# Kernel optimization log

Hardware: AMD Instinct MI355X
Metric: run time of the kernel (lower is better)

## Reference

```python
import jax, jax.numpy as jnp
import numpy as np

# CIN config: input_dim (num_fields) = 32, cross_layer_sizes = [128, 128, 128], split_half = True
NUM_FIELDS = 32
EMBED_DIM = 16
BATCH = 4096
CROSS_SIZES = [128, 128, 128]


def setup_inputs() -> dict:
    key = jax.random.key(0)
    ks = jax.random.split(key, 8)
    x = jax.random.normal(ks[0], (BATCH, NUM_FIELDS, EMBED_DIM), dtype=jnp.float32)
    # Conv1d(kernel_size=1) weights: (out_ch, in_ch) + bias (out_ch,)
    prev = NUM_FIELDS
    inp = {"x": x}
    for i, cs in enumerate(CROSS_SIZES):
        in_ch = NUM_FIELDS * prev
        scale = 1.0 / np.sqrt(in_ch)
        inp[f"W{i}"] = jax.random.uniform(ks[1 + 2 * i], (cs, in_ch), dtype=jnp.float32, minval=-scale, maxval=scale)
        inp[f"b{i}"] = jax.random.uniform(ks[2 + 2 * i], (cs,), dtype=jnp.float32, minval=-scale, maxval=scale)
        prev = cs // 2  # split_half (applied after all but last, but prev for next conv uses halved size)
    return inp


def _cin_forward(x, Ws, bs):
    # x: (B, F, E)
    x0 = x
    h = x
    xs = []
    n_layers = len(Ws)
    for i in range(n_layers):
        B, F, E = x0.shape
        G = h.shape[1]
        # outer product over field dims -> (B, F*G, E)
        z = (x0[:, :, None, :] * h[:, None, :, :]).reshape(B, F * G, E)
        # 1x1 conv == channel matmul; bias broadcast over embed dim; relu
        y = jax.nn.relu(jnp.einsum('oc,bce->boe', Ws[i], z) + bs[i][None, :, None])
        if i != n_layers - 1:
            half = y.shape[1] // 2
            x_keep, h = y[:, :half, :], y[:, half:, :]
        else:
            x_keep, h = y, y
        xs.append(x_keep)
    return jnp.sum(jnp.concatenate(xs, axis=1), axis=2)  # (B, fc_input_dim)


def reference(x, W0, b0, W1, b1, W2, b2):
    return _cin_forward(x, [W0, W1, W2], [b0, b1, b2])
```

## Files before the change

kernel.cpp:

```cpp
#include <hip/hip_runtime.h>

typedef _Float16 half_t;
typedef _Float16 v8h __attribute__((ext_vector_type(8)));
typedef _Float16 v4h __attribute__((ext_vector_type(4)));
typedef float v4f __attribute__((ext_vector_type(4)));

#define XTP 40
#define HP  72

typedef __attribute__((address_space(3))) unsigned int lds_u32;
typedef const __attribute__((address_space(1))) unsigned int glb_u32;

__device__ __forceinline__ void dma16(const half_t* g, half_t* l, int lane) {
  __builtin_amdgcn_global_load_lds((glb_u32*)(g + lane * 8), (lds_u32*)(l), 16, 0, 0);
}

#define WAITVM(N) __builtin_amdgcn_s_waitcnt(0xF70 | (N))
#define SCHED0()  __builtin_amdgcn_sched_barrier(0)

__global__ __launch_bounds__(256) void prep_w_all(const float* __restrict__ W0,
                                                  const float* __restrict__ W1,
                                                  const float* __restrict__ W2,
                                                  half_t* __restrict__ w0h,
                                                  half_t* __restrict__ w1h,
                                                  half_t* __restrict__ w2h) {
  int i = blockIdx.x * 256 + threadIdx.x;
  const float* src; half_t* dst; int o, k8, ktot;
  if (i < 16384)      { o = i >> 7;               k8 = i & 127;               src = W0; dst = w0h; ktot = 1024; }
  else if (i < 49152) { int j = i - 16384; o = j >> 8; k8 = j & 255;          src = W1; dst = w1h; ktot = 2048; }
  else                { int j = i - 49152; o = j >> 8; k8 = j & 255;          src = W2; dst = w2h; ktot = 2048; }
  const float* s = src + (size_t)o * ktot + k8 * 8;
  float4 f0 = *(const float4*)s;
  float4 f1 = *(const float4*)(s + 4);
  union { half_t h[8]; uint4 u; } pk;
  pk.h[0] = (half_t)f0.x; pk.h[1] = (half_t)f0.y; pk.h[2] = (half_t)f0.z; pk.h[3] = (half_t)f0.w;
  pk.h[4] = (half_t)f1.x; pk.h[5] = (half_t)f1.y; pk.h[6] = (half_t)f1.z; pk.h[7] = (half_t)f1.w;
  *(uint4*)(dst + (size_t)(k8 * 128 + o) * 8) = pk.u;
}

template <int G, int NSEL, bool TAIL>
__device__ __forceinline__ void run_quad(const half_t* __restrict__ wgt, int sbase,
                                         half_t* (&r)[4], int wv, int lane, int arow,
                                         const half_t* __restrict__ xt_lds, const int (&lrow)[4],
                                         const v8h (&hreg)[4][NSEL], v4f (&acc)[2][4]) {
  v8h xv8[4]; v4h xv4[4];
  if (G == 64) {
#pragma unroll
    for (int ni = 0; ni < 4; ++ni) xv4[ni] = *(const v4h*)(xt_lds + lrow[ni] * XTP + (sbase >> 1));
  } else {
#pragma unroll
    for (int ni = 0; ni < 4; ++ni) xv8[ni] = *(const v8h*)(xt_lds + lrow[ni] * XTP + sbase);
  }
#pragma unroll
  for (int i = 0; i < 8; ++i) {
    SCHED0();
    if (!TAIL || i <= 5) { WAITVM(2); } else if (i == 6) { WAITVM(1); } else { WAITVM(0); }
    __builtin_amdgcn_s_barrier();
    SCHED0();
    if (!TAIL || i <= 4)
      dma16(wgt + (size_t)(sbase + i + 3) * 4096 + wv * 512, r[3] + wv * 512, lane);
    const int sel = (G == 64) ? (i & 1) : 0;
    v8h a0 = *(const v8h*)(r[0] + arow);
    v8h a1 = *(const v8h*)(r[0] + arow + 128);
    v8h bfr[4];
#pragma unroll
    for (int ni = 0; ni < 4; ++ni) {
      half_t xs = (G == 64) ? xv4[ni][i >> 1] : xv8[ni][i];
      bfr[ni] = hreg[ni][sel] * xs;
    }
#pragma unroll
    for (int ni = 0; ni < 4; ++ni)
      acc[0][ni] = __builtin_amdgcn_mfma_f32_16x16x32_f16(a0, bfr[ni], acc[0][ni], 0, 0, 0);
#pragma unroll
    for (int ni = 0; ni < 4; ++ni)
      acc[1][ni] = __builtin_amdgcn_mfma_f32_16x16x32_f16(a1, bfr[ni], acc[1][ni], 0, 0, 0);
    half_t* t = r[0]; r[0] = r[1]; r[1] = r[2]; r[2] = r[3]; r[3] = t;
  }
}

template <int G, int KTOT, int KEEP, int OUT_BASE, bool H_OUT, bool H_IS_X>
__device__ __forceinline__ void layer(const half_t* __restrict__ wgt,
                                      const float* __restrict__ bias,
                                      half_t* __restrict__ xt_lds,
                                      half_t* __restrict__ h_lds,
                                      half_t* __restrict__ w_ring,
                                      float* __restrict__ out,
                                      size_t b0, int tid) {
  constexpr int NS = KTOT / 32;
  constexpr int NQ = NS / 8;
  constexpr int NSEL = (G == 64) ? 2 : 1;
  const int lane = tid & 63;
  const int wv = tid >> 6;
  const int wm = (wv & 3) * 32;
  const int wb = (wv >> 2) * 4;
  const int col = lane & 15;
  const int kq = lane >> 4;
  const int arow = (kq * 128 + wm + col) * 8;

  int lrow[4];
#pragma unroll
  for (int ni = 0; ni < 4; ++ni) lrow[ni] = (wb + ni) * 16 + col;

  __syncthreads();

  const half_t* hb = H_IS_X ? xt_lds : h_lds;
  const int hpitch = H_IS_X ? XTP : HP;
  v8h hreg[4][NSEL];
#pragma unroll
  for (int ni = 0; ni < 4; ++ni) {
    const half_t* hp = hb + lrow[ni] * hpitch + kq * 8;
    hreg[ni][0] = *(const v8h*)hp;
    if (NSEL > 1) hreg[ni][NSEL - 1] = *(const v8h*)(hp + 32);
  }

#pragma unroll
  for (int p = 0; p < 3; ++p)
    dma16(wgt + (size_t)p * 4096 + wv * 512, w_ring + p * 4096 + wv * 512, lane);

  half_t* r[4] = {w_ring, w_ring + 4096, w_ring + 8192, w_ring + 12288};
  v4f acc[2][4] = {};

#pragma unroll 1
  for (int q = 0; q < NQ - 1; ++q)
    run_quad<G, NSEL, false>(wgt, q * 8, r, wv, lane, arow, xt_lds, lrow, hreg, acc);
  run_quad<G, NSEL, true>(wgt, (NQ - 1) * 8, r, wv, lane, arow, xt_lds, lrow, hreg, acc);

#pragma unroll
  for (int mi = 0; mi < 2; ++mi) {
    const int o_base = wm + mi * 16 + kq * 4;
    float4 b4 = *(const float4*)(bias + o_base);
#pragma unroll
    for (int ni = 0; ni < 4; ++ni) {
      const int bb = wb + ni;
      float v[4];
#pragma unroll
      for (int r2 = 0; r2 < 4; ++r2)
        v[r2] = fmaxf(acc[mi][ni][r2] + (&b4.x)[r2], 0.0f);
      if (H_OUT && o_base >= 64) {
        union { half_t h[4]; uint2 u; } pk;
#pragma unroll
        for (int r2 = 0; r2 < 4; ++r2) pk.h[r2] = (half_t)v[r2];
        *(uint2*)(h_lds + (bb * 16 + col) * HP + (o_base - 64)) = pk.u;
      }
      if (o_base < KEEP) {
#pragma unroll
        for (int r2 = 0; r2 < 4; ++r2) {
          float sv = v[r2];
          sv += __shfl_xor(sv, 1);
          sv += __shfl_xor(sv, 2);
          sv += __shfl_xor(sv, 4);
          sv += __shfl_xor(sv, 8);
          if (col == 0) out[(b0 + bb) * 256 + OUT_BASE + o_base + r2] = sv;
        }
      }
    }
  }
}

__global__ __launch_bounds__(512, 4) void cin_fused(const float* __restrict__ x,
                                                    const half_t* __restrict__ w0h,
                                                    const half_t* __restrict__ w1h,
                                                    const half_t* __restrict__ w2h,
                                                    const float* __restrict__ b0p,
                                                    const float* __restrict__ b1p,
                                                    const float* __restrict__ b2p,
                                                    float* __restrict__ out) {
  __shared__ __align__(16) half_t xt_lds[128 * XTP];
  __shared__ __align__(16) half_t h_lds[128 * HP];
  __shared__ __align__(16) half_t w_ring[4 * 4096];

  const int tid = threadIdx.x;
  const size_t b0 = (size_t)blockIdx.x * 8;

#pragma unroll
  for (int i = 0; i < 2; ++i) {
    int idx = (i * 512 + tid) * 4;
    float4 v = *(const float4*)(x + b0 * 512 + idx);
    int e = idx & 15, f = (idx >> 4) & 31, b = idx >> 9;
    half_t* d = xt_lds + (b * 16 + e) * XTP + f;
    d[0 * XTP] = (half_t)v.x;
    d[1 * XTP] = (half_t)v.y;
    d[2 * XTP] = (half_t)v.z;
    d[3 * XTP] = (half_t)v.w;
  }

  layer<32, 1024, 64, 0, true, true>(w0h, b0p, xt_lds, h_lds, w_ring, out, b0, tid);
  layer<64, 2048, 64, 64, true, false>(w1h, b1p, xt_lds, h_lds, w_ring, out, b0, tid);
  layer<64, 2048, 128, 128, false, false>(w2h, b2p, xt_lds, h_lds, w_ring, out, b0, tid);
}

extern "C" void kernel_launch(void* const* d_in, const int* in_sizes, int n_in,
                              void* d_out, int out_size, void* d_ws, size_t ws_size,
                              hipStream_t stream) {
  const float* x  = (const float*)d_in[0];
  const float* W0 = (const float*)d_in[1];
  const float* b0 = (const float*)d_in[2];
  const float* W1 = (const float*)d_in[3];
  const float* b1 = (const float*)d_in[4];
  const float* W2 = (const float*)d_in[5];
  const float* b2 = (const float*)d_in[6];
  float* out = (float*)d_out;
  char* ws = (char*)d_ws;

  half_t* w0h = (half_t*)(ws);
  half_t* w1h = (half_t*)(ws + (256u << 10));
  half_t* w2h = (half_t*)(ws + (768u << 10));

  prep_w_all<<<320, 256, 0, stream>>>(W0, W1, W2, w0h, w1h, w2h);
  cin_fused<<<512, 512, 0, stream>>>(x, w0h, w1h, w2h, b0, b1, b2, out);
}
```

Before: 153.1 us.

## Use per-wave private weight rings to drop block-wide barriers in K loop

Rearranges the fp16 weight layout so that each group of 32 output rows per K-step is contiguous. Each wave then DMAs only its own 1024-element weight slice into a private 3-deep LDS ring, which removes the per-step s_barrier across all 8 waves. The cost is that the two waves sharing the same output rows each load the same weights, doubling global/L2 weight traffic. LDS for the ring also grows from 4x4096 to 8x3072 halves, which may affect occupancy.

```diff
diff --git a/kernel.cpp b/kernel.cpp
--- a/kernel.cpp
+++ b/kernel.cpp
@@ -26,21 +26,22 @@
                                                   half_t* __restrict__ w2h) {
   int i = blockIdx.x * 256 + threadIdx.x;
   const float* src; half_t* dst; int o, k8, ktot;
-  if (i < 16384)      { o = i >> 7;               k8 = i & 127;               src = W0; dst = w0h; ktot = 1024; }
-  else if (i < 49152) { int j = i - 16384; o = j >> 8; k8 = j & 255;          src = W1; dst = w1h; ktot = 2048; }
-  else                { int j = i - 49152; o = j >> 8; k8 = j & 255;          src = W2; dst = w2h; ktot = 2048; }
+  if (i < 16384)      { o = i >> 7;               k8 = i & 127;      src = W0; dst = w0h; ktot = 1024; }
+  else if (i < 49152) { int j = i - 16384; o = j >> 8; k8 = j & 255; src = W1; dst = w1h; ktot = 2048; }
+  else                { int j = i - 49152; o = j >> 8; k8 = j & 255; src = W2; dst = w2h; ktot = 2048; }
   const float* s = src + (size_t)o * ktot + k8 * 8;
   float4 f0 = *(const float4*)s;
   float4 f1 = *(const float4*)(s + 4);
   union { half_t h[8]; uint4 u; } pk;
   pk.h[0] = (half_t)f0.x; pk.h[1] = (half_t)f0.y; pk.h[2] = (half_t)f0.z; pk.h[3] = (half_t)f0.w;
   pk.h[4] = (half_t)f1.x; pk.h[5] = (half_t)f1.y; pk.h[6] = (half_t)f1.z; pk.h[7] = (half_t)f1.w;
-  *(uint4*)(dst + (size_t)(k8 * 128 + o) * 8) = pk.u;
+  int st = k8 >> 2, kl = k8 & 3, g = o >> 5, ol = o & 31;
+  *(uint4*)(dst + (size_t)((st * 4 + g) * 128 + kl * 32 + ol) * 8) = pk.u;
 }
 
 template <int G, int NSEL, bool TAIL>
-__device__ __forceinline__ void run_quad(const half_t* __restrict__ wgt, int sbase,
-                                         half_t* (&r)[4], int wv, int lane, int arow,
+__device__ __forceinline__ void run_oct8(const half_t* __restrict__ wslice, int sbase,
+                                         half_t* (&rr)[3], int lane, int aoff,
                                          const half_t* __restrict__ xt_lds, const int (&lrow)[4],
                                          const v8h (&hreg)[4][NSEL], v4f (&acc)[2][4]) {
   v8h xv8[4]; v4h xv4[4];
@@ -54,14 +55,17 @@
 #pragma unroll
   for (int i = 0; i < 8; ++i) {
     SCHED0();
-    if (!TAIL || i <= 5) { WAITVM(2); } else if (i == 6) { WAITVM(1); } else { WAITVM(0); }
-    __builtin_amdgcn_s_barrier();
+    if (!TAIL || i < 6) {
+      const half_t* src = wslice + (size_t)(sbase + i + 2) * 4096;
+      dma16(src, rr[2], lane);
+      dma16(src + 512, rr[2] + 512, lane);
+    }
     SCHED0();
-    if (!TAIL || i <= 4)
-      dma16(wgt + (size_t)(sbase + i + 3) * 4096 + wv * 512, r[3] + wv * 512, lane);
+    if (!TAIL || i < 6) { WAITVM(4); } else if (i == 6) { WAITVM(2); } else { WAITVM(0); }
+    SCHED0();
+    v8h a0 = *(const v8h*)(rr[0] + aoff);
+    v8h a1 = *(const v8h*)(rr[0] + aoff + 128);
     const int sel = (G == 64) ? (i & 1) : 0;
-    v8h a0 = *(const v8h*)(r[0] + arow);
-    v8h a1 = *(const v8h*)(r[0] + arow + 128);
     v8h bfr[4];
 #pragma unroll
     for (int ni = 0; ni < 4; ++ni) {
@@ -74,7 +78,7 @@
 #pragma unroll
     for (int ni = 0; ni < 4; ++ni)
       acc[1][ni] = __builtin_amdgcn_mfma_f32_16x16x32_f16(a1, bfr[ni], acc[1][ni], 0, 0, 0);
-    half_t* t = r[0]; r[0] = r[1]; r[1] = r[2]; r[2] = r[3]; r[3] = t;
+    half_t* t0 = rr[0]; rr[0] = rr[1]; rr[1] = rr[2]; rr[2] = t0;
   }
 }
 
@@ -87,7 +91,7 @@
                                       float* __restrict__ out,
                                       size_t b0, int tid) {
   constexpr int NS = KTOT / 32;
-  constexpr int NQ = NS / 8;
+  constexpr int NO8 = NS / 8;
   constexpr int NSEL = (G == 64) ? 2 : 1;
   const int lane = tid & 63;
   const int wv = tid >> 6;
@@ -95,7 +99,8 @@
   const int wb = (wv >> 2) * 4;
   const int col = lane & 15;
   const int kq = lane >> 4;
-  const int arow = (kq * 128 + wm + col) * 8;
+  const int aoff = (kq * 32 + col) * 8;
+  const half_t* wslice = wgt + (wv & 3) * 1024;
 
   int lrow[4];
 #pragma unroll
@@ -113,17 +118,21 @@
     if (NSEL > 1) hreg[ni][NSEL - 1] = *(const v8h*)(hp + 32);
   }
 
-#pragma unroll
-  for (int p = 0; p < 3; ++p)
-    dma16(wgt + (size_t)p * 4096 + wv * 512, w_ring + p * 4096 + wv * 512, lane);
-
-  half_t* r[4] = {w_ring, w_ring + 4096, w_ring + 8192, w_ring + 12288};
+  half_t* base = w_ring + wv * 3072;
+  half_t* rr[3] = {base, base + 1024, base + 2048};
+
+#pragma unroll
+  for (int p = 0; p < 2; ++p) {
+    const half_t* src = wslice + (size_t)p * 4096;
+    dma16(src, rr[p], lane);
+    dma16(src + 512, rr[p] + 512, lane);
+  }
+
   v4f acc[2][4] = {};
-
 #pragma unroll 1
-  for (int q = 0; q < NQ - 1; ++q)
-    run_quad<G, NSEL, false>(wgt, q * 8, r, wv, lane, arow, xt_lds, lrow, hreg, acc);
-  run_quad<G, NSEL, true>(wgt, (NQ - 1) * 8, r, wv, lane, arow, xt_lds, lrow, hreg, acc);
+  for (int oi = 0; oi < NO8 - 1; ++oi)
+    run_oct8<G, NSEL, false>(wslice, oi * 8, rr, lane, aoff, xt_lds, lrow, hreg, acc);
+  run_oct8<G, NSEL, true>(wslice, (NO8 - 1) * 8, rr, lane, aoff, xt_lds, lrow, hreg, acc);
 
 #pragma unroll
   for (int mi = 0; mi < 2; ++mi) {
@@ -167,7 +176,7 @@
                                                     float* __restrict__ out) {
   __shared__ __align__(16) half_t xt_lds[128 * XTP];
   __shared__ __align__(16) half_t h_lds[128 * HP];
-  __shared__ __align__(16) half_t w_ring[4 * 4096];
+  __shared__ __align__(16) half_t w_ring[8 * 3072];
 
   const int tid = threadIdx.x;
   const size_t b0 = (size_t)blockIdx.x * 8;
```

Result: slower. 177.1 us (+15.7%).

## Split K across two wave groups with 16-batch blocks and larger per-wave tiles

Applied to the files above, without the earlier changes.

Blocks grow to 1024 threads covering 16 batch rows, and the waves split into two K-halves, each streaming its own half of the weights through a separate LDS ring. Each wave now computes a 64x64 output tile with 4x4 MFMA accumulators, reusing each B fragment across more A rows. The two K-halves' partial sums are combined through LDS with extra barriers before the epilogue. This halves the number of blocks reading the weights and raises MFMA reuse, at the cost of more accumulator registers, more LDS and a cross-group reduction.

```diff
diff --git a/kernel.cpp b/kernel.cpp
--- a/kernel.cpp
+++ b/kernel.cpp
@@ -26,9 +26,9 @@
                                                   half_t* __restrict__ w2h) {
   int i = blockIdx.x * 256 + threadIdx.x;
   const float* src; half_t* dst; int o, k8, ktot;
-  if (i < 16384)      { o = i >> 7;               k8 = i & 127;               src = W0; dst = w0h; ktot = 1024; }
-  else if (i < 49152) { int j = i - 16384; o = j >> 8; k8 = j & 255;          src = W1; dst = w1h; ktot = 2048; }
-  else                { int j = i - 49152; o = j >> 8; k8 = j & 255;          src = W2; dst = w2h; ktot = 2048; }
+  if (i < 16384)      { o = i >> 7;               k8 = i & 127;      src = W0; dst = w0h; ktot = 1024; }
+  else if (i < 49152) { int j = i - 16384; o = j >> 8; k8 = j & 255; src = W1; dst = w1h; ktot = 2048; }
+  else                { int j = i - 49152; o = j >> 8; k8 = j & 255; src = W2; dst = w2h; ktot = 2048; }
   const float* s = src + (size_t)o * ktot + k8 * 8;
   float4 f0 = *(const float4*)s;
   float4 f1 = *(const float4*)(s + 4);
@@ -39,17 +39,17 @@
 }
 
 template <int G, int NSEL, bool TAIL>
-__device__ __forceinline__ void run_quad(const half_t* __restrict__ wgt, int sbase,
-                                         half_t* (&r)[4], int wv, int lane, int arow,
-                                         const half_t* __restrict__ xt_lds, const int (&lrow)[4],
-                                         const v8h (&hreg)[4][NSEL], v4f (&acc)[2][4]) {
+__device__ __forceinline__ void quad8(const half_t* __restrict__ wbase, half_t* __restrict__ ring,
+                                      int dmaofs, int sbase, int lane, int aoff,
+                                      const half_t* __restrict__ xt_lds, int fofs, const int (&lrow)[4],
+                                      const v8h (&hreg)[4][NSEL], v4f (&acc)[4][4]) {
   v8h xv8[4]; v4h xv4[4];
   if (G == 64) {
 #pragma unroll
-    for (int ni = 0; ni < 4; ++ni) xv4[ni] = *(const v4h*)(xt_lds + lrow[ni] * XTP + (sbase >> 1));
+    for (int ni = 0; ni < 4; ++ni) xv4[ni] = *(const v4h*)(xt_lds + lrow[ni] * XTP + fofs + (sbase >> 1));
   } else {
 #pragma unroll
-    for (int ni = 0; ni < 4; ++ni) xv8[ni] = *(const v8h*)(xt_lds + lrow[ni] * XTP + sbase);
+    for (int ni = 0; ni < 4; ++ni) xv8[ni] = *(const v8h*)(xt_lds + lrow[ni] * XTP + fofs + sbase);
   }
 #pragma unroll
   for (int i = 0; i < 8; ++i) {
@@ -58,23 +58,23 @@
     __builtin_amdgcn_s_barrier();
     SCHED0();
     if (!TAIL || i <= 4)
-      dma16(wgt + (size_t)(sbase + i + 3) * 4096 + wv * 512, r[3] + wv * 512, lane);
+      dma16(wbase + (size_t)(sbase + i + 3) * 4096 + dmaofs,
+            ring + ((i + 3) & 3) * 4096 + dmaofs, lane);
+    const half_t* rb = ring + (i & 3) * 4096;
     const int sel = (G == 64) ? (i & 1) : 0;
-    v8h a0 = *(const v8h*)(r[0] + arow);
-    v8h a1 = *(const v8h*)(r[0] + arow + 128);
-    v8h bfr[4];
+    v8h a[4], bfr[4];
+#pragma unroll
+    for (int mi = 0; mi < 4; ++mi) a[mi] = *(const v8h*)(rb + aoff + mi * 128);
 #pragma unroll
     for (int ni = 0; ni < 4; ++ni) {
       half_t xs = (G == 64) ? xv4[ni][i >> 1] : xv8[ni][i];
       bfr[ni] = hreg[ni][sel] * xs;
     }
 #pragma unroll
-    for (int ni = 0; ni < 4; ++ni)
-      acc[0][ni] = __builtin_amdgcn_mfma_f32_16x16x32_f16(a0, bfr[ni], acc[0][ni], 0, 0, 0);
-#pragma unroll
-    for (int ni = 0; ni < 4; ++ni)
-      acc[1][ni] = __builtin_amdgcn_mfma_f32_16x16x32_f16(a1, bfr[ni], acc[1][ni], 0, 0, 0);
-    half_t* t = r[0]; r[0] = r[1]; r[1] = r[2]; r[2] = r[3]; r[3] = t;
+    for (int mi = 0; mi < 4; ++mi)
+#pragma unroll
+      for (int ni = 0; ni < 4; ++ni)
+        acc[mi][ni] = __builtin_amdgcn_mfma_f32_16x16x32_f16(a[mi], bfr[ni], acc[mi][ni], 0, 0, 0);
   }
 }
 
@@ -86,16 +86,22 @@
                                       half_t* __restrict__ w_ring,
                                       float* __restrict__ out,
                                       size_t b0, int tid) {
-  constexpr int NS = KTOT / 32;
-  constexpr int NQ = NS / 8;
+  constexpr int NSH = KTOT / 64;
+  constexpr int NQ = NSH / 8;
   constexpr int NSEL = (G == 64) ? 2 : 1;
   const int lane = tid & 63;
   const int wv = tid >> 6;
-  const int wm = (wv & 3) * 32;
-  const int wb = (wv >> 2) * 4;
+  const int ks = wv >> 3;
+  const int wq = wv & 7;
+  const int wm = (wq & 1) * 64;
+  const int wb = (wq >> 1) * 4;
   const int col = lane & 15;
   const int kq = lane >> 4;
-  const int arow = (kq * 128 + wm + col) * 8;
+  const int aoff = (kq * 128 + wm + col) * 8;
+  const int fofs = ks * 16;
+  const half_t* wbase = wgt + (size_t)ks * NSH * 4096;
+  half_t* ring = w_ring + ks * 16384;
+  const int dmaofs = wq * 512;
 
   int lrow[4];
 #pragma unroll
@@ -115,18 +121,35 @@
 
 #pragma unroll
   for (int p = 0; p < 3; ++p)
-    dma16(wgt + (size_t)p * 4096 + wv * 512, w_ring + p * 4096 + wv * 512, lane);
-
-  half_t* r[4] = {w_ring, w_ring + 4096, w_ring + 8192, w_ring + 12288};
-  v4f acc[2][4] = {};
-
+    dma16(wbase + (size_t)p * 4096 + dmaofs, ring + p * 4096 + dmaofs, lane);
+
+  v4f acc[4][4] = {};
 #pragma unroll 1
   for (int q = 0; q < NQ - 1; ++q)
-    run_quad<G, NSEL, false>(wgt, q * 8, r, wv, lane, arow, xt_lds, lrow, hreg, acc);
-  run_quad<G, NSEL, true>(wgt, (NQ - 1) * 8, r, wv, lane, arow, xt_lds, lrow, hreg, acc);
-
-#pragma unroll
-  for (int mi = 0; mi < 2; ++mi) {
+    quad8<G, NSEL, false>(wbase, ring, dmaofs, q * 8, lane, aoff, xt_lds, fofs, lrow, hreg, acc);
+  quad8<G, NSEL, true>(wbase, ring, dmaofs, (NQ - 1) * 8, lane, aoff, xt_lds, fofs, lrow, hreg, acc);
+
+  float* scr = (float*)w_ring;
+  float* my = scr + (wq * 64 + lane) * 20;
+#pragma unroll
+  for (int r = 0; r < 4; ++r) {
+    const int row = (r < 2) ? (2 + r) : (r - 2);
+    const int wks = (r < 2) ? 0 : 1;
+    __syncthreads();
+    if (ks == wks) {
+#pragma unroll
+      for (int q2 = 0; q2 < 4; ++q2) *(v4f*)(my + q2 * 4) = acc[row][q2];
+    }
+    __syncthreads();
+    if (ks != wks) {
+#pragma unroll
+      for (int q2 = 0; q2 < 4; ++q2) acc[row][q2] += *(const v4f*)(my + q2 * 4);
+    }
+  }
+
+#pragma unroll
+  for (int ml = 0; ml < 2; ++ml) {
+    const int mi = ks * 2 + ml;
     const int o_base = wm + mi * 16 + kq * 4;
     float4 b4 = *(const float4*)(bias + o_base);
 #pragma unroll
@@ -157,24 +180,24 @@
   }
 }
 
-__global__ __launch_bounds__(512, 4) void cin_fused(const float* __restrict__ x,
-                                                    const half_t* __restrict__ w0h,
-                                                    const half_t* __restrict__ w1h,
-                                                    const half_t* __restrict__ w2h,
-                                                    const float* __restrict__ b0p,
-                                                    const float* __restrict__ b1p,
-                                                    const float* __restrict__ b2p,
-                                                    float* __restrict__ out) {
-  __shared__ __align__(16) half_t xt_lds[128 * XTP];
-  __shared__ __align__(16) half_t h_lds[128 * HP];
-  __shared__ __align__(16) half_t w_ring[4 * 4096];
+__global__ __launch_bounds__(1024, 4) void cin_fused(const float* __restrict__ x,
+                                                     const half_t* __restrict__ w0h,
+                                                     const half_t* __restrict__ w1h,
+                                                     const half_t* __restrict__ w2h,
+                                                     const float* __restrict__ b0p,
+                                                     const float* __restrict__ b1p,
+                                                     const float* __restrict__ b2p,
+                                                     float* __restrict__ out) {
+  __shared__ __align__(16) half_t xt_lds[256 * XTP];
+  __shared__ __align__(16) half_t h_lds[256 * HP];
+  __shared__ __align__(16) half_t w_ring[32768];
 
   const int tid = threadIdx.x;
-  const size_t b0 = (size_t)blockIdx.x * 8;
+  const size_t b0 = (size_t)blockIdx.x * 16;
 
 #pragma unroll
   for (int i = 0; i < 2; ++i) {
-    int idx = (i * 512 + tid) * 4;
+    int idx = (i * 1024 + tid) * 4;
     float4 v = *(const float4*)(x + b0 * 512 + idx);
     int e = idx & 15, f = (idx >> 4) & 31, b = idx >> 9;
     half_t* d = xt_lds + (b * 16 + e) * XTP + f;
@@ -207,5 +230,5 @@
   half_t* w2h = (half_t*)(ws + (768u << 10));
 
   prep_w_all<<<320, 256, 0, stream>>>(W0, W1, W2, w0h, w1h, w2h);
-  cin_fused<<<512, 512, 0, stream>>>(x, w0h, w1h, w2h, b0, b1, b2, out);
-}
+  cin_fused<<<256, 1024, 0, stream>>>(x, w0h, w1h, w2h, b0, b1, b2, out);
+}
```

Measured after the change: 293.3 us. 1.92x slower.

## Split K across wave groups with larger per-wave M tiles and LDS reduction

Applied to the files above, without the earlier changes.

Reorders the fp16 weight prep into field-major slabs so each half of the workgroup streams its own K-range. Each group gets a private 3-deep LDS ring that loads 8 KB per step. Each wave now computes a 64x64 tile (4x4 MFMAs per A fetch instead of 2x4), raising A-fragment reuse and cutting barriers per MFMA. The two K-halves are summed through LDS scratch before the epilogue. This adds extra syncs, LDS traffic and larger LDS use (48 KB ring), which may lower occupancy.

```diff
diff --git a/kernel.cpp b/kernel.cpp
--- a/kernel.cpp
+++ b/kernel.cpp
@@ -25,135 +25,192 @@
                                                   half_t* __restrict__ w1h,
                                                   half_t* __restrict__ w2h) {
   int i = blockIdx.x * 256 + threadIdx.x;
-  const float* src; half_t* dst; int o, k8, ktot;
-  if (i < 16384)      { o = i >> 7;               k8 = i & 127;               src = W0; dst = w0h; ktot = 1024; }
-  else if (i < 49152) { int j = i - 16384; o = j >> 8; k8 = j & 255;          src = W1; dst = w1h; ktot = 2048; }
-  else                { int j = i - 49152; o = j >> 8; k8 = j & 255;          src = W2; dst = w2h; ktot = 2048; }
+  const float* src; half_t* dst; int o, k8, ktot, slab, kl;
+  if (i < 16384) {
+    o = i >> 7; k8 = i & 127; src = W0; dst = w0h; ktot = 1024;
+    int f = k8 >> 2; kl = k8 & 3;
+    slab = (f >> 4) * 16 + (f & 15);
+  } else if (i < 49152) {
+    int j = i - 16384; o = j >> 8; k8 = j & 255; src = W1; dst = w1h; ktot = 2048;
+    int f = k8 >> 3, grem = k8 & 7, sel = grem >> 2; kl = grem & 3;
+    slab = ((f >> 4) * 2 + sel) * 16 + (f & 15);
+  } else {
+    int j = i - 49152; o = j >> 8; k8 = j & 255; src = W2; dst = w2h; ktot = 2048;
+    int f = k8 >> 3, grem = k8 & 7, sel = grem >> 2; kl = grem & 3;
+    slab = ((f >> 4) * 2 + sel) * 16 + (f & 15);
+  }
   const float* s = src + (size_t)o * ktot + k8 * 8;
   float4 f0 = *(const float4*)s;
   float4 f1 = *(const float4*)(s + 4);
   union { half_t h[8]; uint4 u; } pk;
   pk.h[0] = (half_t)f0.x; pk.h[1] = (half_t)f0.y; pk.h[2] = (half_t)f0.z; pk.h[3] = (half_t)f0.w;
   pk.h[4] = (half_t)f1.x; pk.h[5] = (half_t)f1.y; pk.h[6] = (half_t)f1.z; pk.h[7] = (half_t)f1.w;
-  *(uint4*)(dst + (size_t)(k8 * 128 + o) * 8) = pk.u;
-}
-
-template <int G, int NSEL, bool TAIL>
-__device__ __forceinline__ void run_quad(const half_t* __restrict__ wgt, int sbase,
-                                         half_t* (&r)[4], int wv, int lane, int arow,
-                                         const half_t* __restrict__ xt_lds, const int (&lrow)[4],
-                                         const v8h (&hreg)[4][NSEL], v4f (&acc)[2][4]) {
-  v8h xv8[4]; v4h xv4[4];
-  if (G == 64) {
-#pragma unroll
-    for (int ni = 0; ni < 4; ++ni) xv4[ni] = *(const v4h*)(xt_lds + lrow[ni] * XTP + (sbase >> 1));
-  } else {
-#pragma unroll
-    for (int ni = 0; ni < 4; ++ni) xv8[ni] = *(const v8h*)(xt_lds + lrow[ni] * XTP + sbase);
-  }
-#pragma unroll
-  for (int i = 0; i < 8; ++i) {
+  *(uint4*)(dst + (size_t)(slab * 512 + kl * 128 + o) * 8) = pk.u;
+}
+
+template <int S0, bool TAIL>
+__device__ __forceinline__ void quad4(const half_t* __restrict__ pbase, half_t* __restrict__ ringh,
+                                      int dmaofs, int lane, int aoff,
+                                      const half_t* __restrict__ xt_lds, int fbase,
+                                      const int (&lrow)[4], const v8h (&hreg)[4], v4f (&acc)[4][4]) {
+  v4h xv[4];
+#pragma unroll
+  for (int ni = 0; ni < 4; ++ni)
+    xv[ni] = *(const v4h*)(xt_lds + lrow[ni] * XTP + fbase + S0);
+#pragma unroll
+  for (int i = 0; i < 4; ++i) {
     SCHED0();
-    if (!TAIL || i <= 5) { WAITVM(2); } else if (i == 6) { WAITVM(1); } else { WAITVM(0); }
+    if (!TAIL || i < 3) { WAITVM(2); } else { WAITVM(0); }
     __builtin_amdgcn_s_barrier();
     SCHED0();
-    if (!TAIL || i <= 4)
-      dma16(wgt + (size_t)(sbase + i + 3) * 4096 + wv * 512, r[3] + wv * 512, lane);
-    const int sel = (G == 64) ? (i & 1) : 0;
-    v8h a0 = *(const v8h*)(r[0] + arow);
-    v8h a1 = *(const v8h*)(r[0] + arow + 128);
-    v8h bfr[4];
+    if (!TAIL || i <= 1) {
+      const half_t* wsrc = pbase + (size_t)(S0 + i + 2) * 4096 + dmaofs;
+      half_t* wdst = ringh + ((S0 + i + 2) % 3) * 4096 + dmaofs;
+      dma16(wsrc, wdst, lane);
+      dma16(wsrc + 512, wdst + 512, lane);
+    }
+    const half_t* rb = ringh + ((S0 + i) % 3) * 4096;
+    v8h a[4];
+#pragma unroll
+    for (int mi = 0; mi < 4; ++mi) a[mi] = *(const v8h*)(rb + aoff + mi * 128);
 #pragma unroll
     for (int ni = 0; ni < 4; ++ni) {
-      half_t xs = (G == 64) ? xv4[ni][i >> 1] : xv8[ni][i];
-      bfr[ni] = hreg[ni][sel] * xs;
-    }
-#pragma unroll
-    for (int ni = 0; ni < 4; ++ni)
-      acc[0][ni] = __builtin_amdgcn_mfma_f32_16x16x32_f16(a0, bfr[ni], acc[0][ni], 0, 0, 0);
-#pragma unroll
-    for (int ni = 0; ni < 4; ++ni)
-      acc[1][ni] = __builtin_amdgcn_mfma_f32_16x16x32_f16(a1, bfr[ni], acc[1][ni], 0, 0, 0);
-    half_t* t = r[0]; r[0] = r[1]; r[1] = r[2]; r[2] = r[3]; r[3] = t;
-  }
-}
-
-template <int G, int KTOT, int KEEP, int OUT_BASE, bool H_OUT, bool H_IS_X>
-__device__ __forceinline__ void layer(const half_t* __restrict__ wgt,
-                                      const float* __restrict__ bias,
-                                      half_t* __restrict__ xt_lds,
-                                      half_t* __restrict__ h_lds,
-                                      half_t* __restrict__ w_ring,
-                                      float* __restrict__ out,
+      v8h bfr = hreg[ni] * xv[ni][i];
+#pragma unroll
+      for (int mi = 0; mi < 4; ++mi)
+        acc[mi][ni] = __builtin_amdgcn_mfma_f32_16x16x32_f16(a[mi], bfr, acc[mi][ni], 0, 0, 0);
+    }
+  }
+}
+
+__device__ __forceinline__ void run_pass(const half_t* __restrict__ pbase, half_t* __restrict__ ringh,
+                                         int dmaofs, int lane, int aoff, int kq,
+                                         const half_t* __restrict__ hb, int hpitch, int selofs,
+                                         const half_t* __restrict__ xt_lds, int fbase,
+                                         const int (&lrow)[4], v4f (&acc)[4][4]) {
+  v8h hreg[4];
+#pragma unroll
+  for (int ni = 0; ni < 4; ++ni)
+    hreg[ni] = *(const v8h*)(hb + lrow[ni] * hpitch + selofs + kq * 8);
+#pragma unroll
+  for (int p = 0; p < 2; ++p) {
+    const half_t* wsrc = pbase + (size_t)p * 4096 + dmaofs;
+    half_t* wdst = ringh + p * 4096 + dmaofs;
+    dma16(wsrc, wdst, lane);
+    dma16(wsrc + 512, wdst + 512, lane);
+  }
+  quad4<0, false>(pbase, ringh, dmaofs, lane, aoff, xt_lds, fbase, lrow, hreg, acc);
+  quad4<4, false>(pbase, ringh, dmaofs, lane, aoff, xt_lds, fbase, lrow, hreg, acc);
+  quad4<8, false>(pbase, ringh, dmaofs, lane, aoff, xt_lds, fbase, lrow, hreg, acc);
+  quad4<12, true>(pbase, ringh, dmaofs, lane, aoff, xt_lds, fbase, lrow, hreg, acc);
+}
+
+template <int MI, int KEEP, int OUT_BASE, bool H_OUT>
+__device__ __forceinline__ void epi_row(v4f (&acc)[4][4], const float* __restrict__ bias,
+                                        half_t* __restrict__ h_lds, float* __restrict__ out,
+                                        size_t b0, int wm, int wb, int col, int kq) {
+  const int o_base = wm + MI * 16 + kq * 4;
+  float4 b4 = *(const float4*)(bias + o_base);
+#pragma unroll
+  for (int ni = 0; ni < 4; ++ni) {
+    const int bb = wb + ni;
+    float v[4];
+#pragma unroll
+    for (int r2 = 0; r2 < 4; ++r2)
+      v[r2] = fmaxf(acc[MI][ni][r2] + (&b4.x)[r2], 0.0f);
+    if (H_OUT && o_base >= 64) {
+      union { half_t h[4]; uint2 u; } pk;
+#pragma unroll
+      for (int r2 = 0; r2 < 4; ++r2) pk.h[r2] = (half_t)v[r2];
+      *(uint2*)(h_lds + (bb * 16 + col) * HP + (o_base - 64)) = pk.u;
+    }
+    if (o_base < KEEP) {
+#pragma unroll
+      for (int r2 = 0; r2 < 4; ++r2) {
+        float sv = v[r2];
+        sv += __shfl_xor(sv, 1);
+        sv += __shfl_xor(sv, 2);
+        sv += __shfl_xor(sv, 4);
+        sv += __shfl_xor(sv, 8);
+        if (col == 0) out[(b0 + bb) * 256 + OUT_BASE + o_base + r2] = sv;
+      }
+    }
+  }
+}
+
+template <int G, int KEEP, int OUT_BASE, bool H_OUT, bool H_IS_X>
+__device__ __forceinline__ void layer(const half_t* __restrict__ wgt, const float* __restrict__ bias,
+                                      half_t* __restrict__ xt_lds, half_t* __restrict__ h_lds,
+                                      half_t* __restrict__ w_ring, float* __restrict__ out,
                                       size_t b0, int tid) {
-  constexpr int NS = KTOT / 32;
-  constexpr int NQ = NS / 8;
   constexpr int NSEL = (G == 64) ? 2 : 1;
   const int lane = tid & 63;
   const int wv = tid >> 6;
-  const int wm = (wv & 3) * 32;
-  const int wb = (wv >> 2) * 4;
+  const int ks = wv >> 2;
+  const int wm = (wv & 1) * 64;
+  const int nb = ((wv >> 1) & 1) * 4;
   const int col = lane & 15;
   const int kq = lane >> 4;
-  const int arow = (kq * 128 + wm + col) * 8;
+  const int aoff = (kq * 128 + wm + col) * 8;
+  const int dmaofs = (wv & 3) * 1024;
+  half_t* ringh = w_ring + ks * 12288;
+  const int fbase = ks * 16;
 
   int lrow[4];
 #pragma unroll
-  for (int ni = 0; ni < 4; ++ni) lrow[ni] = (wb + ni) * 16 + col;
-
-  __syncthreads();
+  for (int ni = 0; ni < 4; ++ni) lrow[ni] = (nb + ni) * 16 + col;
 
   const half_t* hb = H_IS_X ? xt_lds : h_lds;
   const int hpitch = H_IS_X ? XTP : HP;
-  v8h hreg[4][NSEL];
-#pragma unroll
-  for (int ni = 0; ni < 4; ++ni) {
-    const half_t* hp = hb + lrow[ni] * hpitch + kq * 8;
-    hreg[ni][0] = *(const v8h*)hp;
-    if (NSEL > 1) hreg[ni][NSEL - 1] = *(const v8h*)(hp + 32);
-  }
-
-#pragma unroll
-  for (int p = 0; p < 3; ++p)
-    dma16(wgt + (size_t)p * 4096 + wv * 512, w_ring + p * 4096 + wv * 512, lane);
-
-  half_t* r[4] = {w_ring, w_ring + 4096, w_ring + 8192, w_ring + 12288};
-  v4f acc[2][4] = {};
-
-#pragma unroll 1
-  for (int q = 0; q < NQ - 1; ++q)
-    run_quad<G, NSEL, false>(wgt, q * 8, r, wv, lane, arow, xt_lds, lrow, hreg, acc);
-  run_quad<G, NSEL, true>(wgt, (NQ - 1) * 8, r, wv, lane, arow, xt_lds, lrow, hreg, acc);
-
-#pragma unroll
-  for (int mi = 0; mi < 2; ++mi) {
-    const int o_base = wm + mi * 16 + kq * 4;
-    float4 b4 = *(const float4*)(bias + o_base);
-#pragma unroll
-    for (int ni = 0; ni < 4; ++ni) {
-      const int bb = wb + ni;
-      float v[4];
-#pragma unroll
-      for (int r2 = 0; r2 < 4; ++r2)
-        v[r2] = fmaxf(acc[mi][ni][r2] + (&b4.x)[r2], 0.0f);
-      if (H_OUT && o_base >= 64) {
-        union { half_t h[4]; uint2 u; } pk;
-#pragma unroll
-        for (int r2 = 0; r2 < 4; ++r2) pk.h[r2] = (half_t)v[r2];
-        *(uint2*)(h_lds + (bb * 16 + col) * HP + (o_base - 64)) = pk.u;
-      }
-      if (o_base < KEEP) {
-#pragma unroll
-        for (int r2 = 0; r2 < 4; ++r2) {
-          float sv = v[r2];
-          sv += __shfl_xor(sv, 1);
-          sv += __shfl_xor(sv, 2);
-          sv += __shfl_xor(sv, 4);
-          sv += __shfl_xor(sv, 8);
-          if (col == 0) out[(b0 + bb) * 256 + OUT_BASE + o_base + r2] = sv;
-        }
-      }
-    }
+
+  v4f acc[4][4] = {};
+
+  __syncthreads();
+  run_pass(wgt + (size_t)(ks * NSEL) * 65536, ringh, dmaofs, lane, aoff, kq,
+           hb, hpitch, 0, xt_lds, fbase, lrow, acc);
+  if (NSEL == 2) {
+    __syncthreads();
+    run_pass(wgt + (size_t)(ks * 2 + 1) * 65536, ringh, dmaofs, lane, aoff, kq,
+             hb, hpitch, 32, xt_lds, fbase, lrow, acc);
+  }
+
+  float* scr = (float*)w_ring;
+  float* my = scr + (wv & 3) * 2048 + lane * 4;
+  __syncthreads();
+  if (ks == 0) {
+    *(v4f*)(my + 0 * 256) = acc[2][0]; *(v4f*)(my + 1 * 256) = acc[2][1];
+    *(v4f*)(my + 2 * 256) = acc[2][2]; *(v4f*)(my + 3 * 256) = acc[2][3];
+    *(v4f*)(my + 4 * 256) = acc[3][0]; *(v4f*)(my + 5 * 256) = acc[3][1];
+    *(v4f*)(my + 6 * 256) = acc[3][2]; *(v4f*)(my + 7 * 256) = acc[3][3];
+  }
+  __syncthreads();
+  if (ks == 1) {
+    acc[2][0] += *(const v4f*)(my + 0 * 256); acc[2][1] += *(const v4f*)(my + 1 * 256);
+    acc[2][2] += *(const v4f*)(my + 2 * 256); acc[2][3] += *(const v4f*)(my + 3 * 256);
+    acc[3][0] += *(const v4f*)(my + 4 * 256); acc[3][1] += *(const v4f*)(my + 5 * 256);
+    acc[3][2] += *(const v4f*)(my + 6 * 256); acc[3][3] += *(const v4f*)(my + 7 * 256);
+  }
+  __syncthreads();
+  if (ks == 1) {
+    *(v4f*)(my + 0 * 256) = acc[0][0]; *(v4f*)(my + 1 * 256) = acc[0][1];
+    *(v4f*)(my + 2 * 256) = acc[0][2]; *(v4f*)(my + 3 * 256) = acc[0][3];
+    *(v4f*)(my + 4 * 256) = acc[1][0]; *(v4f*)(my + 5 * 256) = acc[1][1];
+    *(v4f*)(my + 6 * 256) = acc[1][2]; *(v4f*)(my + 7 * 256) = acc[1][3];
+  }
+  __syncthreads();
+  if (ks == 0) {
+    acc[0][0] += *(const v4f*)(my + 0 * 256); acc[0][1] += *(const v4f*)(my + 1 * 256);
+    acc[0][2] += *(const v4f*)(my + 2 * 256); acc[0][3] += *(const v4f*)(my + 3 * 256);
+    acc[1][0] += *(const v4f*)(my + 4 * 256); acc[1][1] += *(const v4f*)(my + 5 * 256);
+    acc[1][2] += *(const v4f*)(my + 6 * 256); acc[1][3] += *(const v4f*)(my + 7 * 256);
+  }
+
+  if (ks == 0) {
+    epi_row<0, KEEP, OUT_BASE, H_OUT>(acc, bias, h_lds, out, b0, wm, nb, col, kq);
+    epi_row<1, KEEP, OUT_BASE, H_OUT>(acc, bias, h_lds, out, b0, wm, nb, col, kq);
+  } else {
+    epi_row<2, KEEP, OUT_BASE, H_OUT>(acc, bias, h_lds, out, b0, wm, nb, col, kq);
+    epi_row<3, KEEP, OUT_BASE, H_OUT>(acc, bias, h_lds, out, b0, wm, nb, col, kq);
   }
 }
 
@@ -167,7 +224,7 @@
                                                     float* __restrict__ out) {
   __shared__ __align__(16) half_t xt_lds[128 * XTP];
   __shared__ __align__(16) half_t h_lds[128 * HP];
-  __shared__ __align__(16) half_t w_ring[4 * 4096];
+  __shared__ __align__(16) half_t w_ring[24576];
 
   const int tid = threadIdx.x;
   const size_t b0 = (size_t)blockIdx.x * 8;
@@ -184,9 +241,9 @@
     d[3 * XTP] = (half_t)v.w;
   }
 
-  layer<32, 1024, 64, 0, true, true>(w0h, b0p, xt_lds, h_lds, w_ring, out, b0, tid);
-  layer<64, 2048, 64, 64, true, false>(w1h, b1p, xt_lds, h_lds, w_ring, out, b0, tid);
-  layer<64, 2048, 128, 128, false, false>(w2h, b2p, xt_lds, h_lds, w_ring, out, b0, tid);
+  layer<32, 64, 0, true, true>(w0h, b0p, xt_lds, h_lds, w_ring, out, b0, tid);
+  layer<64, 64, 64, true, false>(w1h, b1p, xt_lds, h_lds, w_ring, out, b0, tid);
+  layer<64, 128, 128, false, false>(w2h, b2p, xt_lds, h_lds, w_ring, out, b0, tid);
 }
 
 extern "C" void kernel_launch(void* const* d_in, const int* in_sizes, int n_in,
```

New measurement: 153.4 us. No clear change (+0.1%).
